# Kernel tuning notes

Measured on AMD Instinct MI355X. Metric: run time of the kernel, lower is better.

The kernel has to match this reference:

```python
import jax, jax.numpy as jnp
import numpy as np

N, E = 50000, 600000
IN_DIM, HID, OUT_DIM = 128, 256, 64


def _sage_conv(x, edge_index, W_l, W_r, b):
    # PyG SAGEConv (mean aggr, root_weight=True):
    # out = mean_{j in N(i)} x_j @ W_l + x_i @ W_r + b
    src, dst = edge_index[0], edge_index[1]
    msg = x[src]  # [E, d] gather
    agg = jax.ops.segment_sum(msg, dst, num_segments=N)  # [N, d]
    cnt = jax.ops.segment_sum(jnp.ones((E,), dtype=x.dtype), dst, num_segments=N)
    agg = agg / jnp.maximum(cnt, 1.0)[:, None]
    return agg @ W_l + x @ W_r + b


def setup_inputs() -> dict:
    key = jax.random.key(0)
    ks = jax.random.split(key, 8)
    x = jax.random.normal(ks[0], (N, IN_DIM), dtype=jnp.float32)
    edge_index = jax.random.randint(ks[1], (2, E), 0, N, dtype=jnp.int64)
    s1 = 1.0 / np.sqrt(IN_DIM)
    s2 = 1.0 / np.sqrt(HID)
    W1_l = jax.random.uniform(ks[2], (IN_DIM, HID), jnp.float32, -s1, s1)
    W1_r = jax.random.uniform(ks[3], (IN_DIM, HID), jnp.float32, -s1, s1)
    b1 = jnp.zeros((HID,), jnp.float32)
    W2_l = jax.random.uniform(ks[4], (HID, OUT_DIM), jnp.float32, -s2, s2)
    W2_r = jax.random.uniform(ks[5], (HID, OUT_DIM), jnp.float32, -s2, s2)
    b2 = jnp.zeros((OUT_DIM,), jnp.float32)
    return {"x": x, "edge_index": edge_index, "W1_l": W1_l, "W1_r": W1_r,
            "b1": b1, "W2_l": W2_l, "W2_r": W2_r, "b2": b2}


def reference(x, edge_index, W1_l, W1_r, b1, W2_l, W2_r, b2):
    # SAGE.forward, eval mode (dropout = identity)
    h = jax.nn.relu(_sage_conv(x, edge_index, W1_l, W1_r, b1))
    out = _sage_conv(h, edge_index, W2_l, W2_r, b2)
    return out
```

## Files before the change

### kernel.cpp

```cpp
#include <hip/hip_runtime.h>

#define N_NODES 50000
#define N_EDGES 600000
#define N_PAD   50048
#define IN_DIM 128
#define HID 256
#define OUT_DIM 64
#define MAX_DEG 64

typedef __attribute__((ext_vector_type(4))) float f32x4;
typedef __attribute__((ext_vector_type(8))) short short8;
typedef unsigned short u16;
typedef unsigned int u32;

__device__ __forceinline__ float bf2f(u32 lo16) {
  u32 u = lo16 << 16;
  return __builtin_bit_cast(float, u);
}
__device__ __forceinline__ u16 f2bf(float f) {
  u32 u = __builtin_bit_cast(u32, f);
  u = (u + 0x7FFF + ((u >> 16) & 1)) >> 16;
  return (u16)u;
}

#define SEG0 (N_PAD * 16)
#define SEG1 (SEG0 + 256 * 256)
#define SEG2 (SEG1 + 128 * 256)
#define SEG3 (SEG2 + N_NODES)
#define PREP_TOT SEG3

__global__ void k_prep(const float* __restrict__ x,
                       const float* __restrict__ W1l, const float* __restrict__ W1r,
                       const float* __restrict__ W2l, const float* __restrict__ W2r,
                       u16* __restrict__ Abig, u16* __restrict__ W1t,
                       u16* __restrict__ W2t, int* __restrict__ cnt) {
  int idx = blockIdx.x * 256 + threadIdx.x;
  if (idx < SEG0) {
    int row = idx >> 4;
    int c8 = (idx & 15) * 8;
    short8 o;
    if (row < N_NODES) {
      f32x4 a = *(const f32x4*)&x[(size_t)row * 128 + c8];
      f32x4 b = *(const f32x4*)&x[(size_t)row * 128 + c8 + 4];
      o[0] = (short)f2bf(a[0]); o[1] = (short)f2bf(a[1]);
      o[2] = (short)f2bf(a[2]); o[3] = (short)f2bf(a[3]);
      o[4] = (short)f2bf(b[0]); o[5] = (short)f2bf(b[1]);
      o[6] = (short)f2bf(b[2]); o[7] = (short)f2bf(b[3]);
    } else {
      for (int j = 0; j < 8; ++j) o[j] = 0;
    }
    *(short8*)&Abig[(size_t)row * 256 + 128 + c8] = o;
  } else if (idx < SEG1) {
    int i = idx - SEG0;
    int nn = i >> 8, k = i & 255;
    float v = (k < 128) ? W1l[(size_t)k * HID + nn] : W1r[(size_t)(k - 128) * HID + nn];
    W1t[(size_t)nn * 256 + k] = f2bf(v);
  } else if (idx < SEG2) {
    int i = idx - SEG1;
    int nn = i >> 8, k = i & 255;
    float v = (nn < 64) ? W2l[(size_t)k * OUT_DIM + nn]
                        : W2r[(size_t)k * OUT_DIM + (nn - 64)];
    W2t[(size_t)nn * 256 + k] = f2bf(v);
  } else if (idx < SEG3) {
    cnt[idx - SEG2] = 0;
  }
}


__global__ void k_fill(const int* __restrict__ src, const int* __restrict__ dst,
                       int* __restrict__ cnt, int* __restrict__ bucket) {
  int e = blockIdx.x * 256 + threadIdx.x;
  if (e < N_EDGES) {
    int d = dst[e];
    int pos = atomicAdd(&cnt[d], 1);
    if (pos < MAX_DEG) bucket[(size_t)d * MAX_DEG + pos] = src[e];
  }
}


__global__ void k_agg(const u16* __restrict__ Ax, const int* __restrict__ cnt,
                      const int* __restrict__ bucket, u16* __restrict__ Aagg) {
  int node = blockIdx.x * 4 + (threadIdx.x >> 6);
  if (node >= N_PAD) return;
  int lane = threadIdx.x & 63;
  int es = lane >> 4, dl = lane & 15;
  int deg = (node < N_NODES) ? cnt[node] : 0;
  int sreg = (node < N_NODES) ? bucket[(size_t)node * MAX_DEG + lane] : 0;
  float acc[8] = {0.f, 0.f, 0.f, 0.f, 0.f, 0.f, 0.f, 0.f};
  for (int e = 0; e < deg; e += 4) {
    int ee = e + es;
    int s = __shfl(sreg, ee & 63);
    if (ee < deg) {
      short8 v = *(const short8*)&Ax[(size_t)s * 256 + 128 + dl * 8];
#pragma unroll
      for (int j = 0; j < 8; ++j) acc[j] += bf2f((u16)v[j]);
    }
  }
#pragma unroll
  for (int j = 0; j < 8; ++j) {
    acc[j] += __shfl_xor(acc[j], 16);
    acc[j] += __shfl_xor(acc[j], 32);
  }
  float inv = 1.f / fmaxf((float)deg, 1.f);
  if (es == 0) {
    short8 o;
#pragma unroll
    for (int j = 0; j < 8; ++j) o[j] = (short)f2bf(acc[j] * inv);
    *(short8*)&Aagg[(size_t)node * 256 + dl * 8] = o;
  }
}


__device__ __forceinline__ void gl_lds16(const void* g, void* l) {
  __builtin_amdgcn_global_load_lds((const __attribute__((address_space(1))) u32*)g,
                                   (__attribute__((address_space(3))) u32*)l, 16, 0, 0);
}

template <int BM, int RELU, int OSTRIDE>
__global__ __launch_bounds__(256) void k_gemm(
    const u16* __restrict__ A, const u16* __restrict__ Bt,
    const float* __restrict__ bias, u16* __restrict__ C) {
  constexpr int M_REP = BM / 32;
  constexpr int ACH = BM / 32;
  __shared__ u16 As[2][BM * 64];
  __shared__ u16 Bs[2][128 * 64];
  const int t = threadIdx.x;
  const int wave = t >> 6;
  const int lane = t & 63;
  const int brow = blockIdx.x * BM;
  const int bcol = blockIdx.y * 128;
  const int wr = (wave >> 1) * (BM / 2);
  const int wc = (wave & 1) * 64;
  const int lr = lane & 15;
  const int kg = lane >> 4;

  f32x4 acc[M_REP][4];
#pragma unroll
  for (int m = 0; m < M_REP; ++m)
#pragma unroll
    for (int n = 0; n < 4; ++n) acc[m][n] = (f32x4){0.f, 0.f, 0.f, 0.f};

  auto stage = [&](int buf, int kt) {
    const int k0 = kt * 64;
#pragma unroll
    for (int i = 0; i < ACH; ++i) {
      int chunk = wave * ACH + i;
      int f = chunk * 1024 + lane * 16;
      int row = f >> 7;
      int cbs = (f & 127) ^ ((row & 7) << 4);
      gl_lds16(&A[(size_t)(brow + row) * 256 + k0 + (cbs >> 1)],
               (char*)As[buf] + chunk * 1024);
    }
#pragma unroll
    for (int i = 0; i < 4; ++i) {
      int chunk = wave * 4 + i;
      int f = chunk * 1024 + lane * 16;
      int row = f >> 7;
      int cbs = (f & 127) ^ ((row & 7) << 4);
      gl_lds16(&Bt[(size_t)(bcol + row) * 256 + k0 + (cbs >> 1)],
               (char*)Bs[buf] + chunk * 1024);
    }
  };

  stage(0, 0);
  __syncthreads();

#pragma unroll
  for (int kt = 0; kt < 4; ++kt) {
    const int cur = kt & 1;
    if (kt < 3) stage(cur ^ 1, kt + 1);
#pragma unroll
    for (int kk = 0; kk < 2; ++kk) {
      short8 af[M_REP], bfr[4];
      const int cb = kk * 64 + kg * 16;
#pragma unroll
      for (int m = 0; m < M_REP; ++m) {
        int row = wr + m * 16 + lr;
        af[m] = *(const short8*)((const char*)As[cur] + row * 128 + (cb ^ ((row & 7) << 4)));
      }
#pragma unroll
      for (int n = 0; n < 4; ++n) {
        int row = wc + n * 16 + lr;
        bfr[n] = *(const short8*)((const char*)Bs[cur] + row * 128 + (cb ^ ((row & 7) << 4)));
      }
#pragma unroll
      for (int m = 0; m < M_REP; ++m)
#pragma unroll
        for (int n = 0; n < 4; ++n)
          acc[m][n] =
              __builtin_amdgcn_mfma_f32_16x16x32_bf16(af[m], bfr[n], acc[m][n], 0, 0, 0);
    }
    if (kt < 3) __syncthreads();
  }

  const int r0 = brow + wr + kg * 4;
  const int c0 = bcol + wc + lr;
#pragma unroll
  for (int n = 0; n < 4; ++n) {
    int col = c0 + n * 16;
    float bv = 0.f;
    if (RELU) bv = bias[col];
#pragma unroll
    for (int m = 0; m < M_REP; ++m) {
#pragma unroll
      for (int j = 0; j < 4; ++j) {
        int row = r0 + m * 16 + j;
        float v = acc[m][n][j] + bv;
        if (RELU) v = fmaxf(v, 0.f);
        C[(size_t)row * OSTRIDE + col] = f2bf(v);
      }
    }
  }
}


__global__ void k_out(const u16* __restrict__ pq, const int* __restrict__ cnt,
                      const int* __restrict__ bucket, const float* __restrict__ b2,
                      float* __restrict__ out) {
  int node = blockIdx.x * 4 + (threadIdx.x >> 6);
  if (node >= N_NODES) return;
  int lane = threadIdx.x & 63;
  int es = lane >> 3, dl = lane & 7;
  int deg = cnt[node];
  int sreg = bucket[(size_t)node * MAX_DEG + lane];
  float acc[8] = {0.f, 0.f, 0.f, 0.f, 0.f, 0.f, 0.f, 0.f};
  for (int e = 0; e < deg; e += 8) {
    int ee = e + es;
    int s = __shfl(sreg, ee & 63);
    if (ee < deg) {
      short8 v = *(const short8*)&pq[(size_t)s * 128 + dl * 8];
#pragma unroll
      for (int j = 0; j < 8; ++j) acc[j] += bf2f((u16)v[j]);
    }
  }
#pragma unroll
  for (int j = 0; j < 8; ++j) {
    acc[j] += __shfl_xor(acc[j], 8);
    acc[j] += __shfl_xor(acc[j], 16);
    acc[j] += __shfl_xor(acc[j], 32);
  }
  float inv = 1.f / fmaxf((float)deg, 1.f);
  if (es == 0) {
    short8 q = *(const short8*)&pq[(size_t)node * 128 + 64 + dl * 8];
    f32x4 bb0 = *(const f32x4*)&b2[dl * 8];
    f32x4 bb1 = *(const f32x4*)&b2[dl * 8 + 4];
    f32x4 o0, o1;
#pragma unroll
    for (int j = 0; j < 4; ++j) {
      o0[j] = acc[j] * inv + bf2f((u16)q[j]) + bb0[j];
      o1[j] = acc[j + 4] * inv + bf2f((u16)q[j + 4]) + bb1[j];
    }
    *(f32x4*)&out[(size_t)node * 64 + dl * 8] = o0;
    *(f32x4*)&out[(size_t)node * 64 + dl * 8 + 4] = o1;
  }
}


extern "C" void kernel_launch(void* const* d_in, const int* in_sizes, int n_in,
                              void* d_out, int out_size, void* d_ws, size_t ws_size,
                              hipStream_t stream) {
  const float* x   = (const float*)d_in[0];
  const int*   ei  = (const int*)d_in[1];
  const float* W1l = (const float*)d_in[2];
  const float* W1r = (const float*)d_in[3];
  const float* b1  = (const float*)d_in[4];
  const float* W2l = (const float*)d_in[5];
  const float* W2r = (const float*)d_in[6];
  const float* b2  = (const float*)d_in[7];
  float* out = (float*)d_out;

  const int* src = ei;
  const int* dst = ei + N_EDGES;

  char* ws = (char*)d_ws;
  size_t off = 0;
  auto alloc = [&](size_t bytes) -> void* {
    void* p = ws + off;
    off = (off + bytes + 255) & ~(size_t)255;
    return p;
  };
  int* cnt    = (int*)alloc((size_t)N_NODES * 4);
  int* bucket = (int*)alloc((size_t)N_NODES * MAX_DEG * 4);
  u16* Abig   = (u16*)alloc((size_t)N_PAD * 256 * 2);
  u16* W1t    = (u16*)alloc((size_t)256 * 256 * 2);
  u16* W2t    = (u16*)alloc((size_t)128 * 256 * 2);
  u16* h      = (u16*)alloc((size_t)N_PAD * 256 * 2);
  u16* pq     = (u16*)alloc((size_t)N_PAD * 128 * 2);

  k_prep<<<(PREP_TOT + 255) / 256, 256, 0, stream>>>(x, W1l, W1r, W2l, W2r,
                                                     Abig, W1t, W2t, cnt);
  k_fill<<<(N_EDGES + 255) / 256, 256, 0, stream>>>(src, dst, cnt, bucket);
  k_agg<<<N_PAD / 4, 256, 0, stream>>>(Abig, cnt, bucket, Abig);

  k_gemm<128, 1, 256><<<dim3(N_PAD / 128, 2), 256, 0, stream>>>(Abig, W1t, b1, h);
  k_gemm<64, 0, 128><<<dim3(N_PAD / 64, 1), 256, 0, stream>>>(h, W2t, nullptr, pq);

  k_out<<<(N_NODES + 3) / 4, 256, 0, stream>>>(pq, cnt, bucket, b2, out);
}
```

Measured before the change: 121.1 us.

## Fuse both layer GEMMs into one kernel keeping hidden activations in LDS

The two GEMM launches become a single k_mlp kernel. It computes a 64-row tile of the first layer across all 256 hidden columns, applies bias and ReLU, writes the hidden tile into swizzled LDS, and then runs the second GEMM from LDS. This avoids writing and re-reading the N x 256 hidden tensor in global memory and removes one launch. The interleaved Abig buffer is also split into separate xb/agg arrays and the output into separate p/q arrays. In exchange, B tiles for the first GEMM are no longer double-buffered (extra syncs), W2 fragments are read straight from global memory, and LDS use per block grows.

```diff
diff --git a/kernel.cpp b/kernel.cpp
--- a/kernel.cpp
+++ b/kernel.cpp
@@ -32,7 +32,7 @@
 __global__ void k_prep(const float* __restrict__ x,
                        const float* __restrict__ W1l, const float* __restrict__ W1r,
                        const float* __restrict__ W2l, const float* __restrict__ W2r,
-                       u16* __restrict__ Abig, u16* __restrict__ W1t,
+                       u16* __restrict__ xb, u16* __restrict__ W1t,
                        u16* __restrict__ W2t, int* __restrict__ cnt) {
   int idx = blockIdx.x * 256 + threadIdx.x;
   if (idx < SEG0) {
@@ -49,7 +49,7 @@
     } else {
       for (int j = 0; j < 8; ++j) o[j] = 0;
     }
-    *(short8*)&Abig[(size_t)row * 256 + 128 + c8] = o;
+    *(short8*)&xb[(size_t)row * 128 + c8] = o;
   } else if (idx < SEG1) {
     int i = idx - SEG0;
     int nn = i >> 8, k = i & 255;
@@ -78,8 +78,8 @@
 }
 
 
-__global__ void k_agg(const u16* __restrict__ Ax, const int* __restrict__ cnt,
-                      const int* __restrict__ bucket, u16* __restrict__ Aagg) {
+__global__ void k_agg(const u16* __restrict__ xb, const int* __restrict__ cnt,
+                      const int* __restrict__ bucket, u16* __restrict__ agg) {
   int node = blockIdx.x * 4 + (threadIdx.x >> 6);
   if (node >= N_PAD) return;
   int lane = threadIdx.x & 63;
@@ -91,7 +91,7 @@
     int ee = e + es;
     int s = __shfl(sreg, ee & 63);
     if (ee < deg) {
-      short8 v = *(const short8*)&Ax[(size_t)s * 256 + 128 + dl * 8];
+      short8 v = *(const short8*)&xb[(size_t)s * 128 + dl * 8];
 #pragma unroll
       for (int j = 0; j < 8; ++j) acc[j] += bf2f((u16)v[j]);
     }
@@ -106,7 +106,7 @@
     short8 o;
 #pragma unroll
     for (int j = 0; j < 8; ++j) o[j] = (short)f2bf(acc[j] * inv);
-    *(short8*)&Aagg[(size_t)node * 256 + dl * 8] = o;
+    *(short8*)&agg[(size_t)node * 128 + dl * 8] = o;
   }
 }
 
@@ -116,107 +116,156 @@
                                    (__attribute__((address_space(3))) u32*)l, 16, 0, 0);
 }
 
-template <int BM, int RELU, int OSTRIDE>
-__global__ __launch_bounds__(256) void k_gemm(
-    const u16* __restrict__ A, const u16* __restrict__ Bt,
-    const float* __restrict__ bias, u16* __restrict__ C) {
-  constexpr int M_REP = BM / 32;
-  constexpr int ACH = BM / 32;
-  __shared__ u16 As[2][BM * 64];
-  __shared__ u16 Bs[2][128 * 64];
+__global__ __launch_bounds__(256, 2) void k_mlp(
+    const u16* __restrict__ agg, const u16* __restrict__ xb,
+    const u16* __restrict__ W1t, const u16* __restrict__ W2t,
+    const float* __restrict__ b1, u16* __restrict__ pb, u16* __restrict__ qb) {
+  __shared__ u16 hs[64 * 256];
+  __shared__ u16 As[2][64 * 64];
+  __shared__ u16 Bs[256 * 64];
   const int t = threadIdx.x;
   const int wave = t >> 6;
   const int lane = t & 63;
-  const int brow = blockIdx.x * BM;
-  const int bcol = blockIdx.y * 128;
-  const int wr = (wave >> 1) * (BM / 2);
-  const int wc = (wave & 1) * 64;
+  const int brow = blockIdx.x * 64;
   const int lr = lane & 15;
   const int kg = lane >> 4;
 
-  f32x4 acc[M_REP][4];
-#pragma unroll
-  for (int m = 0; m < M_REP; ++m)
-#pragma unroll
-    for (int n = 0; n < 4; ++n) acc[m][n] = (f32x4){0.f, 0.f, 0.f, 0.f};
-
-  auto stage = [&](int buf, int kt) {
-    const int k0 = kt * 64;
-#pragma unroll
-    for (int i = 0; i < ACH; ++i) {
-      int chunk = wave * ACH + i;
+  const int wr = (wave >> 1) * 32;
+  const int wc = (wave & 1) * 128;
+
+  f32x4 acc[2][8];
+#pragma unroll
+  for (int m = 0; m < 2; ++m)
+#pragma unroll
+    for (int n = 0; n < 8; ++n) acc[m][n] = (f32x4){0.f, 0.f, 0.f, 0.f};
+
+  auto stageA = [&](int buf, int kt) {
+    const u16* base = (kt < 2) ? agg : xb;
+    const int koff = (kt & 1) * 64;
+#pragma unroll
+    for (int i = 0; i < 2; ++i) {
+      int chunk = wave * 2 + i;
       int f = chunk * 1024 + lane * 16;
       int row = f >> 7;
       int cbs = (f & 127) ^ ((row & 7) << 4);
-      gl_lds16(&A[(size_t)(brow + row) * 256 + k0 + (cbs >> 1)],
+      gl_lds16(&base[(size_t)(brow + row) * 128 + koff + (cbs >> 1)],
                (char*)As[buf] + chunk * 1024);
     }
-#pragma unroll
-    for (int i = 0; i < 4; ++i) {
-      int chunk = wave * 4 + i;
+  };
+  auto stageB = [&](int kt) {
+    const int k0 = kt * 64;
+#pragma unroll
+    for (int i = 0; i < 8; ++i) {
+      int chunk = wave * 8 + i;
       int f = chunk * 1024 + lane * 16;
       int row = f >> 7;
       int cbs = (f & 127) ^ ((row & 7) << 4);
-      gl_lds16(&Bt[(size_t)(bcol + row) * 256 + k0 + (cbs >> 1)],
-               (char*)Bs[buf] + chunk * 1024);
+      gl_lds16(&W1t[(size_t)row * 256 + k0 + (cbs >> 1)],
+               (char*)Bs + chunk * 1024);
     }
   };
 
-  stage(0, 0);
+  stageA(0, 0);
+  stageB(0);
   __syncthreads();
 
 #pragma unroll
   for (int kt = 0; kt < 4; ++kt) {
     const int cur = kt & 1;
-    if (kt < 3) stage(cur ^ 1, kt + 1);
+    if (kt < 3) stageA(cur ^ 1, kt + 1);
 #pragma unroll
     for (int kk = 0; kk < 2; ++kk) {
-      short8 af[M_REP], bfr[4];
+      short8 af[2], bfr[8];
       const int cb = kk * 64 + kg * 16;
 #pragma unroll
-      for (int m = 0; m < M_REP; ++m) {
+      for (int m = 0; m < 2; ++m) {
         int row = wr + m * 16 + lr;
         af[m] = *(const short8*)((const char*)As[cur] + row * 128 + (cb ^ ((row & 7) << 4)));
       }
 #pragma unroll
-      for (int n = 0; n < 4; ++n) {
+      for (int n = 0; n < 8; ++n) {
         int row = wc + n * 16 + lr;
-        bfr[n] = *(const short8*)((const char*)Bs[cur] + row * 128 + (cb ^ ((row & 7) << 4)));
+        bfr[n] = *(const short8*)((const char*)Bs + row * 128 + (cb ^ ((row & 7) << 4)));
       }
 #pragma unroll
-      for (int m = 0; m < M_REP; ++m)
-#pragma unroll
-        for (int n = 0; n < 4; ++n)
+      for (int m = 0; m < 2; ++m)
+#pragma unroll
+        for (int n = 0; n < 8; ++n)
           acc[m][n] =
               __builtin_amdgcn_mfma_f32_16x16x32_bf16(af[m], bfr[n], acc[m][n], 0, 0, 0);
     }
-    if (kt < 3) __syncthreads();
-  }
-
-  const int r0 = brow + wr + kg * 4;
-  const int c0 = bcol + wc + lr;
+    __syncthreads();
+    if (kt < 3) {
+      stageB(kt + 1);
+      __syncthreads();
+    }
+  }
+
+#pragma unroll
+  for (int n = 0; n < 8; ++n) {
+    int col = wc + n * 16 + lr;
+    float bv = b1[col];
+#pragma unroll
+    for (int m = 0; m < 2; ++m) {
+#pragma unroll
+      for (int j = 0; j < 4; ++j) {
+        int row = wr + kg * 4 + m * 16 + j;
+        float v = fmaxf(acc[m][n][j] + bv, 0.f);
+        *(u16*)((char*)hs + row * 512 + ((col * 2) ^ ((row & 7) << 4))) = f2bf(v);
+      }
+    }
+  }
+  __syncthreads();
+
+  const int wr2 = (wave >> 1) * 32;
+  const int wc2 = (wave & 1) * 64;
+  f32x4 acc2[2][4];
+#pragma unroll
+  for (int m = 0; m < 2; ++m)
+#pragma unroll
+    for (int n = 0; n < 4; ++n) acc2[m][n] = (f32x4){0.f, 0.f, 0.f, 0.f};
+
+#pragma unroll
+  for (int kk = 0; kk < 8; ++kk) {
+    const int cb = kk * 64 + kg * 16;
+    short8 af[2], bfr[4];
+#pragma unroll
+    for (int m = 0; m < 2; ++m) {
+      int row = wr2 + m * 16 + lr;
+      af[m] = *(const short8*)((const char*)hs + row * 512 + (cb ^ ((row & 7) << 4)));
+    }
+#pragma unroll
+    for (int n = 0; n < 4; ++n) {
+      int row = wc2 + n * 16 + lr;
+      bfr[n] = *(const short8*)&W2t[(size_t)row * 256 + kk * 32 + kg * 8];
+    }
+#pragma unroll
+    for (int m = 0; m < 2; ++m)
+#pragma unroll
+      for (int n = 0; n < 4; ++n)
+        acc2[m][n] =
+            __builtin_amdgcn_mfma_f32_16x16x32_bf16(af[m], bfr[n], acc2[m][n], 0, 0, 0);
+  }
+
+  u16* outb = (wave & 1) ? qb : pb;
 #pragma unroll
   for (int n = 0; n < 4; ++n) {
-    int col = c0 + n * 16;
-    float bv = 0.f;
-    if (RELU) bv = bias[col];
-#pragma unroll
-    for (int m = 0; m < M_REP; ++m) {
+    int col = (wc2 + n * 16 + lr) & 63;
+#pragma unroll
+    for (int m = 0; m < 2; ++m) {
 #pragma unroll
       for (int j = 0; j < 4; ++j) {
-        int row = r0 + m * 16 + j;
-        float v = acc[m][n][j] + bv;
-        if (RELU) v = fmaxf(v, 0.f);
-        C[(size_t)row * OSTRIDE + col] = f2bf(v);
+        int row = brow + wr2 + kg * 4 + m * 16 + j;
+        outb[(size_t)row * 64 + col] = f2bf(acc2[m][n][j]);
       }
     }
   }
 }
 
 
-__global__ void k_out(const u16* __restrict__ pq, const int* __restrict__ cnt,
-                      const int* __restrict__ bucket, const float* __restrict__ b2,
-                      float* __restrict__ out) {
+__global__ void k_out(const u16* __restrict__ pb, const u16* __restrict__ qb,
+                      const int* __restrict__ cnt, const int* __restrict__ bucket,
+                      const float* __restrict__ b2, float* __restrict__ out) {
   int node = blockIdx.x * 4 + (threadIdx.x >> 6);
   if (node >= N_NODES) return;
   int lane = threadIdx.x & 63;
@@ -228,7 +277,7 @@
     int ee = e + es;
     int s = __shfl(sreg, ee & 63);
     if (ee < deg) {
-      short8 v = *(const short8*)&pq[(size_t)s * 128 + dl * 8];
+      short8 v = *(const short8*)&pb[(size_t)s * 64 + dl * 8];
 #pragma unroll
       for (int j = 0; j < 8; ++j) acc[j] += bf2f((u16)v[j]);
     }
@@ -241,7 +290,7 @@
   }
   float inv = 1.f / fmaxf((float)deg, 1.f);
   if (es == 0) {
-    short8 q = *(const short8*)&pq[(size_t)node * 128 + 64 + dl * 8];
+    short8 q = *(const short8*)&qb[(size_t)node * 64 + dl * 8];
     f32x4 bb0 = *(const f32x4*)&b2[dl * 8];
     f32x4 bb1 = *(const f32x4*)&b2[dl * 8 + 4];
     f32x4 o0, o1;
@@ -281,19 +330,17 @@
   };
   int* cnt    = (int*)alloc((size_t)N_NODES * 4);
   int* bucket = (int*)alloc((size_t)N_NODES * MAX_DEG * 4);
-  u16* Abig   = (u16*)alloc((size_t)N_PAD * 256 * 2);
+  u16* xb     = (u16*)alloc((size_t)N_PAD * 128 * 2);
+  u16* agg    = (u16*)alloc((size_t)N_PAD * 128 * 2);
   u16* W1t    = (u16*)alloc((size_t)256 * 256 * 2);
   u16* W2t    = (u16*)alloc((size_t)128 * 256 * 2);
-  u16* h      = (u16*)alloc((size_t)N_PAD * 256 * 2);
-  u16* pq     = (u16*)alloc((size_t)N_PAD * 128 * 2);
+  u16* pb     = (u16*)alloc((size_t)N_PAD * 64 * 2);
+  u16* qb     = (u16*)alloc((size_t)N_PAD * 64 * 2);
 
   k_prep<<<(PREP_TOT + 255) / 256, 256, 0, stream>>>(x, W1l, W1r, W2l, W2r,
-                                                     Abig, W1t, W2t, cnt);
+                                                     xb, W1t, W2t, cnt);
   k_fill<<<(N_EDGES + 255) / 256, 256, 0, stream>>>(src, dst, cnt, bucket);
-  k_agg<<<N_PAD / 4, 256, 0, stream>>>(Abig, cnt, bucket, Abig);
-
-  k_gemm<128, 1, 256><<<dim3(N_PAD / 128, 2), 256, 0, stream>>>(Abig, W1t, b1, h);
-  k_gemm<64, 0, 128><<<dim3(N_PAD / 64, 1), 256, 0, stream>>>(h, W2t, nullptr, pq);
-
-  k_out<<<(N_NODES + 3) / 4, 256, 0, stream>>>(pq, cnt, bucket, b2, out);
-}
+  k_agg<<<N_PAD / 4, 256, 0, stream>>>(xb, cnt, bucket, agg);
+  k_mlp<<<N_PAD / 64, 256, 0, stream>>>(agg, xb, W1t, W2t, b1, pb, qb);
+  k_out<<<(N_NODES + 3) / 4, 256, 0, stream>>>(pb, qb, cnt, bucket, b2, out);
+}
```

Result: no change. 121.1 us (-0.0%).
